# Kernel tuning notes

Measured on AMD Instinct MI355X. Metric: run time of the kernel, lower is better.

The kernel has to match this reference:

```python
import jax, jax.numpy as jnp
import numpy as np

N, E, F_IN, H, T, G, NCONV = 50000, 800000, 128, 64, 8, 64, 3
BN_EPS = 1e-5


def _bn_relu(h, gamma, beta):
    # BatchNorm1d in training mode: biased batch stats over the node dim
    m = h.mean(axis=0)
    v = h.var(axis=0)
    return jax.nn.relu(gamma * (h - m) * jax.lax.rsqrt(v + BN_EPS) + beta)


def _mlp(h, W1, b1, g1, be1, W2, b2, g2, be2):
    h = _bn_relu(h @ W1 + b1, g1, be1)
    return _bn_relu(h @ W2 + b2, g2, be2)


def setup_inputs() -> dict:
    key = jax.random.key(0)
    ks = jax.random.split(key, 12)
    x = jax.random.normal(ks[0], (N, F_IN), dtype=jnp.float32)
    edge_index = jax.random.randint(ks[1], (2, E), 0, N, dtype=jnp.int64)
    batch = jnp.sort(jax.random.randint(ks[2], (N,), 0, G, dtype=jnp.int64))
    s = 0.05
    inp = {
        "x": x, "edge_index": edge_index, "batch": batch,
        # first_h: Linear(F_IN,H)+BN+ReLU+Linear(H,H)+BN+ReLU
        "fh_W1": jax.random.normal(ks[3], (F_IN, H), jnp.float32) * s,
        "fh_b1": jnp.zeros((H,), jnp.float32),
        "fh_g1": jnp.ones((H,), jnp.float32),
        "fh_be1": jnp.zeros((H,), jnp.float32),
        "fh_W2": jax.random.normal(ks[4], (H, H), jnp.float32) * s,
        "fh_b2": jnp.zeros((H,), jnp.float32),
        "fh_g2": jnp.ones((H,), jnp.float32),
        "fh_be2": jnp.zeros((H,), jnp.float32),
        # stacked GINConv MLPs (all H->H)
        "cv_W1": jax.random.normal(ks[5], (NCONV, H, H), jnp.float32) * s,
        "cv_b1": jnp.zeros((NCONV, H), jnp.float32),
        "cv_g1": jnp.ones((NCONV, H), jnp.float32),
        "cv_be1": jnp.zeros((NCONV, H), jnp.float32),
        "cv_W2": jax.random.normal(ks[6], (NCONV, H, H), jnp.float32) * s,
        "cv_b2": jnp.zeros((NCONV, H), jnp.float32),
        "cv_g2": jnp.ones((NCONV, H), jnp.float32),
        "cv_be2": jnp.zeros((NCONV, H), jnp.float32),
        # per-layer readout linears (NCONV+1 of them)
        "lin_W": jax.random.normal(ks[7], (NCONV + 1, H, T), jnp.float32) * s,
        "lin_b": jnp.zeros((NCONV + 1, T), jnp.float32),
    }
    return inp


def reference(x, edge_index, batch, fh_W1, fh_b1, fh_g1, fh_be1, fh_W2, fh_b2,
              fh_g2, fh_be2, cv_W1, cv_b1, cv_g1, cv_be1, cv_W2, cv_b2, cv_g2,
              cv_be2, lin_W, lin_b):
    src, dst = edge_index[0], edge_index[1]
    eps = 0.0  # eps=0.0, train_eps=False
    # layer 0: first_h + pooled readout
    h = _mlp(x, fh_W1, fh_b1, fh_g1, fh_be1, fh_W2, fh_b2, fh_g2, fh_be2)
    out = jax.ops.segment_max(h @ lin_W[0] + lin_b[0], batch, num_segments=G)
    # GIN conv layers: neighbor sum-aggregation + MLP, with per-layer readout
    for l in range(NCONV):
        agg = jax.ops.segment_sum(h[src], dst, num_segments=N)  # [N,H]
        h = _mlp((1.0 + eps) * h + agg, cv_W1[l], cv_b1[l], cv_g1[l],
                 cv_be1[l], cv_W2[l], cv_b2[l], cv_g2[l], cv_be2[l])
        out = out + jax.ops.segment_max(h @ lin_W[l + 1] + lin_b[l + 1],
                                        batch, num_segments=G)
    return (out, h)
```

## Files before the change

kernel.cpp:

```cpp
#include <hip/hip_runtime.h>
#include <hip/hip_fp16.h>

#define NN 50000
#define EE 800000
#define FIN 128
#define HH 64
#define TT 8
#define GG 64
#define NCONVS 3
#define BN_EPS 1e-5f
#define RNODES 128
#define NBKT 196
#define SCAT_CHUNK 2048

__device__ __forceinline__ unsigned enc_f32(float x) {
  unsigned u = __float_as_uint(x);
  return (u & 0x80000000u) ? ~u : (u | 0x80000000u);
}
__device__ __forceinline__ float dec_f32(unsigned e) {
  unsigned u = (e & 0x80000000u) ? (e & 0x7fffffffu) : ~e;
  return __uint_as_float(u);
}

template <int K, int MODE>
__global__ __launch_bounds__(256) void mm_stats_kernel(
    const float* __restrict__ in, const __half* __restrict__ hin,
    const float* __restrict__ agg, const float* __restrict__ stats_in,
    const float* __restrict__ gamma, const float* __restrict__ beta,
    const float* __restrict__ W, const float* __restrict__ bias,
    __half* __restrict__ y16, float* __restrict__ stats_out) {
  __shared__ float Wl[K * HH];
  __shared__ float Al[16][K + 1];
  __shared__ float ssl[128];
  __shared__ float sred[4][128];
  const int t = threadIdx.x;
  {
    const float4* W4 = (const float4*)W;
    float4* Wl4 = (float4*)Wl;
#pragma unroll
    for (int i = 0; i < (K * HH) / 1024; ++i) Wl4[t + i * 256] = W4[t + i * 256];
  }
  if (MODE == 1 && t < 64) {
    const float inv = 1.f / (float)NN;
    const float mean = stats_in[t] * inv;
    const float var = stats_in[64 + t] * inv - mean * mean;
    const float sc = gamma[t] * rsqrtf(var + BN_EPS);
    ssl[t] = sc;
    ssl[64 + t] = fmaf(-mean, sc, beta[t]);
  }
  const int r = t >> 4, g = t & 15;
  const float4 bb = *(const float4*)&bias[g * 4];
  float st_s[4] = {0.f, 0.f, 0.f, 0.f}, st_q[4] = {0.f, 0.f, 0.f, 0.f};
  __syncthreads();

#pragma unroll
  for (int chunk = 0; chunk < 4; ++chunk) {
    const int row = blockIdx.x * 64 + chunk * 16 + r;
    if (row < NN) {
      if (MODE == 0) {
#pragma unroll
        for (int p = 0; p < K / 64; ++p) {
          const int c0 = g * 4 + p * 64;
          const float4 v = *(const float4*)&in[row * K + c0];
          Al[r][c0 + 0] = v.x; Al[r][c0 + 1] = v.y;
          Al[r][c0 + 2] = v.z; Al[r][c0 + 3] = v.w;
        }
      } else if (MODE == 1) {
        const int c0 = g * 4;
        const int2 hraw = *(const int2*)&hin[row * HH + c0];
        const float2 f0 = __half22float2(*(const __half2*)&hraw.x);
        const float2 f1 = __half22float2(*(const __half2*)&hraw.y);
        Al[r][c0 + 0] = fmaxf(fmaf(f0.x, ssl[c0 + 0], ssl[64 + c0 + 0]), 0.f);
        Al[r][c0 + 1] = fmaxf(fmaf(f0.y, ssl[c0 + 1], ssl[64 + c0 + 1]), 0.f);
        Al[r][c0 + 2] = fmaxf(fmaf(f1.x, ssl[c0 + 2], ssl[64 + c0 + 2]), 0.f);
        Al[r][c0 + 3] = fmaxf(fmaf(f1.y, ssl[c0 + 3], ssl[64 + c0 + 3]), 0.f);
      } else {
        const int c0 = g * 4;
        const int2 hraw = *(const int2*)&hin[row * HH + c0];
        const float2 f0 = __half22float2(*(const __half2*)&hraw.x);
        const float2 f1 = __half22float2(*(const __half2*)&hraw.y);
        const float4 a = *(const float4*)&agg[row * HH + c0];
        Al[r][c0 + 0] = f0.x + a.x; Al[r][c0 + 1] = f0.y + a.y;
        Al[r][c0 + 2] = f1.x + a.z; Al[r][c0 + 3] = f1.y + a.w;
      }
    } else {
#pragma unroll
      for (int p = 0; p < K / 64; ++p) {
        const int c0 = g * 4 + p * 64;
        Al[r][c0 + 0] = 0.f; Al[r][c0 + 1] = 0.f;
        Al[r][c0 + 2] = 0.f; Al[r][c0 + 3] = 0.f;
      }
    }
    __syncthreads();
    float ax = 0.f, ay = 0.f, az = 0.f, aw = 0.f;
#pragma unroll
    for (int k = 0; k < K; ++k) {
      const float a = Al[r][k];
      const float4 w = *(const float4*)&Wl[k * HH + g * 4];
      ax = fmaf(a, w.x, ax); ay = fmaf(a, w.y, ay);
      az = fmaf(a, w.z, az); aw = fmaf(a, w.w, aw);
    }
    if (row < NN) {
      float4 o;
      o.x = ax + bb.x; o.y = ay + bb.y; o.z = az + bb.z; o.w = aw + bb.w;
      const __half2 p0 = __floats2half2_rn(o.x, o.y);
      const __half2 p1 = __floats2half2_rn(o.z, o.w);
      int2 pk;
      pk.x = *(const int*)&p0; pk.y = *(const int*)&p1;
      *(int2*)&y16[row * HH + g * 4] = pk;
      st_s[0] += o.x; st_s[1] += o.y; st_s[2] += o.z; st_s[3] += o.w;
      st_q[0] = fmaf(o.x, o.x, st_q[0]); st_q[1] = fmaf(o.y, o.y, st_q[1]);
      st_q[2] = fmaf(o.z, o.z, st_q[2]); st_q[3] = fmaf(o.w, o.w, st_q[3]);
    }
    __syncthreads();
  }
#pragma unroll
  for (int off = 16; off <= 32; off <<= 1) {
#pragma unroll
    for (int i = 0; i < 4; ++i) {
      st_s[i] += __shfl_xor(st_s[i], off);
      st_q[i] += __shfl_xor(st_q[i], off);
    }
  }
  const int wave = t >> 6, lane = t & 63;
  if (lane < 16) {
#pragma unroll
    for (int i = 0; i < 4; ++i) {
      sred[wave][lane * 4 + i] = st_s[i];
      sred[wave][64 + lane * 4 + i] = st_q[i];
    }
  }
  __syncthreads();
  if (t < 128)
    atomicAdd(&stats_out[t],
              sred[0][t] + sred[1][t] + sred[2][t] + sred[3][t]);
}

__global__ __launch_bounds__(256) void bcount_kernel(const int* __restrict__ ei,
                                                     int* __restrict__ bcnt) {
  __shared__ int l[256];
  const int t = threadIdx.x;
  l[t] = 0;
  __syncthreads();
  for (int e = blockIdx.x * 256 + t; e < EE; e += gridDim.x * 256)
    atomicAdd(&l[ei[EE + e] >> 8], 1);
  __syncthreads();
  if (t < NBKT && l[t]) atomicAdd(&bcnt[t], l[t]);
}

__global__ void bscan_kernel(const int* __restrict__ bcnt,
                             int* __restrict__ bbase, int* __restrict__ bcur) {
  __shared__ int s[256];
  const int t = threadIdx.x;
  const int v = (t < NBKT) ? bcnt[t] : 0;
  s[t] = v;
  __syncthreads();
  for (int off = 1; off < 256; off <<= 1) {
    const int u = (t >= off) ? s[t - off] : 0;
    __syncthreads();
    s[t] += u;
    __syncthreads();
  }
  const int excl = s[t] - v;
  if (t < NBKT) {
    bbase[t] = excl;
    bcur[t] = excl;
  }
  if (t == 255) bbase[NBKT] = s[255];
}

__global__ __launch_bounds__(256) void bscatter_kernel(
    const int* __restrict__ ei, int* __restrict__ bcur,
    unsigned long long* __restrict__ ebuf) {
  __shared__ int lcnt[256];
  __shared__ int lbase[256];
  const int t = threadIdx.x;
  lcnt[t] = 0;
  __syncthreads();
  const int e0 = blockIdx.x * SCAT_CHUNK;
  int mysrc[8], mydl[8], mybkt[8], myloc[8];
#pragma unroll
  for (int i = 0; i < 8; ++i) {
    const int e = e0 + i * 256 + t;
    if (e < EE) {
      const int dst = ei[EE + e];
      mybkt[i] = dst >> 8;
      mydl[i] = dst & 255;
      mysrc[i] = ei[e];
      myloc[i] = atomicAdd(&lcnt[mybkt[i]], 1);
    } else {
      mybkt[i] = -1;
    }
  }
  __syncthreads();
  if (t < NBKT && lcnt[t]) lbase[t] = atomicAdd(&bcur[t], lcnt[t]);
  __syncthreads();
#pragma unroll
  for (int i = 0; i < 8; ++i) {
    if (mybkt[i] >= 0) {
      const int pos = lbase[mybkt[i]] + myloc[i];
      ebuf[pos] = ((unsigned long long)(unsigned)mydl[i] << 32) |
                  (unsigned)mysrc[i];
    }
  }
}

__global__ __launch_bounds__(256) void bcsr_kernel(
    const int* __restrict__ bbase, const unsigned long long* __restrict__ ebuf,
    int* __restrict__ offs, int* __restrict__ srcs) {
  __shared__ int ldeg[256];
  __shared__ int sscan[256];
  __shared__ int lcur[256];
  const int t = threadIdx.x;
  const int b = blockIdx.x;
  const int e0 = bbase[b], e1 = bbase[b + 1];
  ldeg[t] = 0;
  __syncthreads();
  for (int e = e0 + t; e < e1; e += 256)
    atomicAdd(&ldeg[(int)(ebuf[e] >> 32)], 1);
  __syncthreads();
  const int v = ldeg[t];
  sscan[t] = v;
  __syncthreads();
  for (int off = 1; off < 256; off <<= 1) {
    const int u = (t >= off) ? sscan[t - off] : 0;
    __syncthreads();
    sscan[t] += u;
    __syncthreads();
  }
  const int excl = sscan[t] - v;
  const int node = b * 256 + t;
  if (node < NN) offs[node] = e0 + excl;
  if (b == NBKT - 1 && t == 0) offs[NN] = EE;
  lcur[t] = e0 + excl;
  __syncthreads();
  for (int e = e0 + t; e < e1; e += 256) {
    const unsigned long long u = ebuf[e];
    const int dl = (int)(u >> 32);
    const int pos = atomicAdd(&lcur[dl], 1);
    srcs[pos] = (int)(u & 0xffffffffu);
  }
}

__device__ __forceinline__ void acc_half8(const int4 r, float4& lo, float4& hi) {
  const __half2* p = (const __half2*)&r;
  const float2 f0 = __half22float2(p[0]);
  const float2 f1 = __half22float2(p[1]);
  const float2 f2 = __half22float2(p[2]);
  const float2 f3 = __half22float2(p[3]);
  lo.x += f0.x; lo.y += f0.y; lo.z += f1.x; lo.w += f1.y;
  hi.x += f2.x; hi.y += f2.y; hi.z += f3.x; hi.w += f3.y;
}

__global__ __launch_bounds__(256) void gather16_kernel(
    const int* __restrict__ offs, const int* __restrict__ srcs,
    const __half* __restrict__ h16, float* __restrict__ agg) {
  const int gid = blockIdx.x * 256 + threadIdx.x;
  const int n = gid >> 3, lane = gid & 7;
  if (n >= NN) return;
  const int c0 = lane * 8;
  const int s0 = offs[n], s1 = offs[n + 1];
  float4 aA0 = make_float4(0, 0, 0, 0), aA1 = make_float4(0, 0, 0, 0);
  float4 aB0 = make_float4(0, 0, 0, 0), aB1 = make_float4(0, 0, 0, 0);
  int j = s0;
  for (; j + 1 < s1; j += 2) {
    const int sA = srcs[j], sB = srcs[j + 1];
    const int4 rA = *(const int4*)&h16[sA * HH + c0];
    const int4 rB = *(const int4*)&h16[sB * HH + c0];
    acc_half8(rA, aA0, aA1);
    acc_half8(rB, aB0, aB1);
  }
  if (j < s1) {
    const int4 rA = *(const int4*)&h16[srcs[j] * HH + c0];
    acc_half8(rA, aA0, aA1);
  }
  aA0.x += aB0.x; aA0.y += aB0.y; aA0.z += aB0.z; aA0.w += aB0.w;
  aA1.x += aB1.x; aA1.y += aB1.y; aA1.z += aB1.z; aA1.w += aB1.w;
  *(float4*)&agg[n * HH + c0] = aA0;
  *(float4*)&agg[n * HH + c0 + 4] = aA1;
}

template <int WMODE>
__global__ __launch_bounds__(256) void bnrelu_readout_kernel(
    const __half* __restrict__ y2, const float* __restrict__ stats_in,
    const float* __restrict__ gamma, const float* __restrict__ beta,
    float* __restrict__ hout, __half* __restrict__ h16out,
    const float* __restrict__ linW, const float* __restrict__ linb,
    const int* __restrict__ batch, unsigned* __restrict__ outmax) {
  __shared__ float Wl[HH * 9];
  __shared__ float lb[8];
  __shared__ float ssl[128];
  __shared__ unsigned smax[8][8];
  const int t = threadIdx.x;
  if (t < 64) {
#pragma unroll
    for (int j = 0; j < 8; ++j) Wl[t * 9 + j] = linW[t * 8 + j];
    const float inv = 1.f / (float)NN;
    const float mean = stats_in[t] * inv;
    const float var = stats_in[64 + t] * inv - mean * mean;
    const float sc = gamma[t] * rsqrtf(var + BN_EPS);
    ssl[t] = sc;
    ssl[64 + t] = fmaf(-mean, sc, beta[t]);
  }
  if (t < 8) lb[t] = linb[t];
  if (t >= 64 && t < 128) smax[(t - 64) >> 3][(t - 64) & 7] = 0u;
  const int gfirst = batch[blockIdx.x * RNODES < NN ? blockIdx.x * RNODES : NN - 1];
  __syncthreads();
  const int nl = t >> 3;
  const int c0 = (t & 7) * 8;
  const int b0 = t & 1, b1 = (t >> 1) & 1, b2 = (t >> 2) & 1;
#pragma unroll
  for (int chunk = 0; chunk < RNODES / 32; ++chunk) {
    const int n = blockIdx.x * RNODES + chunk * 32 + nl;
    if (n < NN) {
      float hv[8];
      {
        const int4 rv = *(const int4*)&y2[n * HH + c0];
        const __half2* hp = (const __half2*)&rv;
        const float2 f0 = __half22float2(hp[0]);
        const float2 f1 = __half22float2(hp[1]);
        const float2 f2 = __half22float2(hp[2]);
        const float2 f3 = __half22float2(hp[3]);
        hv[0] = fmaxf(fmaf(f0.x, ssl[c0 + 0], ssl[64 + c0 + 0]), 0.f);
        hv[1] = fmaxf(fmaf(f0.y, ssl[c0 + 1], ssl[64 + c0 + 1]), 0.f);
        hv[2] = fmaxf(fmaf(f1.x, ssl[c0 + 2], ssl[64 + c0 + 2]), 0.f);
        hv[3] = fmaxf(fmaf(f1.y, ssl[c0 + 3], ssl[64 + c0 + 3]), 0.f);
        hv[4] = fmaxf(fmaf(f2.x, ssl[c0 + 4], ssl[64 + c0 + 4]), 0.f);
        hv[5] = fmaxf(fmaf(f2.y, ssl[c0 + 5], ssl[64 + c0 + 5]), 0.f);
        hv[6] = fmaxf(fmaf(f3.x, ssl[c0 + 6], ssl[64 + c0 + 6]), 0.f);
        hv[7] = fmaxf(fmaf(f3.y, ssl[c0 + 7], ssl[64 + c0 + 7]), 0.f);
      }
      if (WMODE == 1) {
        *(float4*)&hout[n * HH + c0] = make_float4(hv[0], hv[1], hv[2], hv[3]);
        *(float4*)&hout[n * HH + c0 + 4] = make_float4(hv[4], hv[5], hv[6], hv[7]);
      } else {
        const __half2 p0 = __floats2half2_rn(hv[0], hv[1]);
        const __half2 p1 = __floats2half2_rn(hv[2], hv[3]);
        const __half2 p2 = __floats2half2_rn(hv[4], hv[5]);
        const __half2 p3 = __floats2half2_rn(hv[6], hv[7]);
        int4 pk;
        pk.x = *(const int*)&p0; pk.y = *(const int*)&p1;
        pk.z = *(const int*)&p2; pk.w = *(const int*)&p3;
        *(int4*)&h16out[n * HH + c0] = pk;
      }
      float rr[8] = {0, 0, 0, 0, 0, 0, 0, 0};
#pragma unroll
      for (int j = 0; j < 8; ++j) {
        const float a = hv[j];
        const int k = c0 + j;
#pragma unroll
        for (int u = 0; u < 8; ++u) rr[u] = fmaf(a, Wl[k * 9 + u], rr[u]);
      }
      float s4[4];
#pragma unroll
      for (int i = 0; i < 4; ++i) {
        const float keepv = b0 ? rr[2 * i + 1] : rr[2 * i];
        const float send = b0 ? rr[2 * i] : rr[2 * i + 1];
        s4[i] = keepv + __shfl_xor(send, 1);
      }
      float s2[2];
#pragma unroll
      for (int i = 0; i < 2; ++i) {
        const float keepv = b1 ? s4[2 * i + 1] : s4[2 * i];
        const float send = b1 ? s4[2 * i] : s4[2 * i + 1];
        s2[i] = keepv + __shfl_xor(send, 2);
      }
      const float keepv = b2 ? s2[1] : s2[0];
      const float send = b2 ? s2[0] : s2[1];
      const float v = keepv + __shfl_xor(send, 4) + lb[t & 7];
      const int g = batch[n];
      const int gidx = g - gfirst;
      const unsigned ev = enc_f32(v);
      if (gidx < 8)
        atomicMax(&smax[gidx][t & 7], ev);
      else
        atomicMax(&outmax[g * 8 + (t & 7)], ev);
    }
  }
  __syncthreads();
  if (t < 64) {
    const unsigned vv = smax[t >> 3][t & 7];
    if (vv) atomicMax(&outmax[(gfirst + (t >> 3)) * 8 + (t & 7)], vv);
  }
}

__global__ void combine_kernel(const unsigned* __restrict__ outmax,
                               float* __restrict__ out) {
  const int i = blockIdx.x * 64 + threadIdx.x;
  float s = 0.f;
#pragma unroll
  for (int l = 0; l < 4; ++l) s += dec_f32(outmax[l * GG * TT + i]);
  out[i] = s;
}

extern "C" void kernel_launch(void* const* d_in, const int* in_sizes, int n_in,
                              void* d_out, int out_size, void* d_ws,
                              size_t ws_size, hipStream_t stream) {
  const float* x      = (const float*)d_in[0];
  const int*   ei     = (const int*)d_in[1];
  const int*   batch  = (const int*)d_in[2];
  const float* fh_W1  = (const float*)d_in[3];
  const float* fh_b1  = (const float*)d_in[4];
  const float* fh_g1  = (const float*)d_in[5];
  const float* fh_be1 = (const float*)d_in[6];
  const float* fh_W2  = (const float*)d_in[7];
  const float* fh_b2  = (const float*)d_in[8];
  const float* fh_g2  = (const float*)d_in[9];
  const float* fh_be2 = (const float*)d_in[10];
  const float* cv_W1  = (const float*)d_in[11];
  const float* cv_b1  = (const float*)d_in[12];
  const float* cv_g1  = (const float*)d_in[13];
  const float* cv_be1 = (const float*)d_in[14];
  const float* cv_W2  = (const float*)d_in[15];
  const float* cv_b2  = (const float*)d_in[16];
  const float* cv_g2  = (const float*)d_in[17];
  const float* cv_be2 = (const float*)d_in[18];
  const float* lin_W  = (const float*)d_in[19];
  const float* lin_b  = (const float*)d_in[20];

  float* out = (float*)d_out;
  float* h = out + GG * TT;

  char* w = (char*)d_ws;
  float* stats = (float*)w;                       w += 8 * 128 * 4;
  unsigned* outmax = (unsigned*)w;                w += 4 * GG * TT * 4;
  int* bcnt = (int*)w;                            w += 256 * 4;
  int* bbase = (int*)w;                           w += 256 * 4;
  int* bcur = (int*)w;                            w += 256 * 4;
  int* offs = (int*)w;                            w += (NN + 1) * 4;
  int* srcs = (int*)w;                            w += (size_t)EE * 4;
  w = (char*)(((size_t)w + 15) & ~(size_t)15);
  __half* h16 = (__half*)w;                       w += (size_t)NN * HH * 2;
  __half* y1 = (__half*)w;                        w += (size_t)NN * HH * 2;
  __half* y2 = (__half*)w;                        w += (size_t)NN * HH * 2;
  w = (char*)(((size_t)w + 15) & ~(size_t)15);
  float* agg = (float*)w;                         w += (size_t)NN * HH * 4;
  unsigned long long* ebuf = (unsigned long long*)agg;

  const int NBLK = (NN + 63) / 64;
  const int NRD = (NN + RNODES - 1) / RNODES;
  const int NGA = (NN * 8 + 255) / 256;
  const int NSC = (EE + SCAT_CHUNK - 1) / SCAT_CHUNK;

  hipMemsetAsync(stats, 0, (8 * 128 + 4 * GG * TT) * sizeof(float), stream);
  hipMemsetAsync(bcnt, 0, 256 * sizeof(int), stream);

  bcount_kernel<<<512, 256, 0, stream>>>(ei, bcnt);
  bscan_kernel<<<1, 256, 0, stream>>>(bcnt, bbase, bcur);
  bscatter_kernel<<<NSC, 256, 0, stream>>>(ei, bcur, ebuf);
  bcsr_kernel<<<NBKT, 256, 0, stream>>>(bbase, ebuf, offs, srcs);

  mm_stats_kernel<FIN, 0><<<NBLK, 256, 0, stream>>>(
      x, nullptr, nullptr, nullptr, nullptr, nullptr, fh_W1, fh_b1, y1, stats);
  mm_stats_kernel<HH, 1><<<NBLK, 256, 0, stream>>>(
      nullptr, y1, nullptr, stats, fh_g1, fh_be1, fh_W2, fh_b2, y2, stats + 128);
  bnrelu_readout_kernel<0><<<NRD, 256, 0, stream>>>(
      y2, stats + 128, fh_g2, fh_be2, h, h16, lin_W, lin_b, batch, outmax);

  for (int l = 0; l < NCONVS; ++l) {
    float* s1 = stats + (2 + 2 * l) * 128;
    float* s2 = stats + (3 + 2 * l) * 128;
    gather16_kernel<<<NGA, 256, 0, stream>>>(offs, srcs, h16, agg);
    mm_stats_kernel<HH, 2><<<NBLK, 256, 0, stream>>>(
        nullptr, h16, agg, nullptr, nullptr, nullptr,
        cv_W1 + l * HH * HH, cv_b1 + l * HH, y1, s1);
    mm_stats_kernel<HH, 1><<<NBLK, 256, 0, stream>>>(
        nullptr, y1, nullptr, s1, cv_g1 + l * HH, cv_be1 + l * HH,
        cv_W2 + l * HH * HH, cv_b2 + l * HH, y2, s2);
    if (l == NCONVS - 1) {
      bnrelu_readout_kernel<1><<<NRD, 256, 0, stream>>>(
          y2, s2, cv_g2 + l * HH, cv_be2 + l * HH, h, h16,
          lin_W + (l + 1) * HH * TT, lin_b + (l + 1) * TT, batch,
          outmax + (l + 1) * GG * TT);
    } else {
      bnrelu_readout_kernel<0><<<NRD, 256, 0, stream>>>(
          y2, s2, cv_g2 + l * HH, cv_be2 + l * HH, h, h16,
          lin_W + (l + 1) * HH * TT, lin_b + (l + 1) * TT, batch,
          outmax + (l + 1) * GG * TT);
    }
  }
  combine_kernel<<<8, 64, 0, stream>>>(outmax, out);
}
```

Before: 407.1 us.

## Register-tile matmul with transposed LDS staging and store aggregation in fp16

The fused matmul+stats kernel now computes a 4x4 output tile per thread. A is staged once per 64-wide K phase into a transposed, padded LDS buffer, which replaces the four 16-row chunks, each with its own barriers and LDS reads. This raises FMA-per-LDS-load reuse and removes most synchronisation. Separately, the neighbour aggregation buffer is written and read as fp16 instead of fp32, halving that round-trip traffic in every conv layer at some cost in accumulation precision.

```diff
diff --git a/kernel.cpp b/kernel.cpp
--- a/kernel.cpp
+++ b/kernel.cpp
@@ -25,94 +25,126 @@
 template <int K, int MODE>
 __global__ __launch_bounds__(256) void mm_stats_kernel(
     const float* __restrict__ in, const __half* __restrict__ hin,
-    const float* __restrict__ agg, const float* __restrict__ stats_in,
+    const __half* __restrict__ agg, const float* __restrict__ stats_in,
     const float* __restrict__ gamma, const float* __restrict__ beta,
     const float* __restrict__ W, const float* __restrict__ bias,
     __half* __restrict__ y16, float* __restrict__ stats_out) {
+  constexpr int NPH = K / 64;
   __shared__ float Wl[K * HH];
-  __shared__ float Al[16][K + 1];
+  __shared__ float AT[64 * 68];
   __shared__ float ssl[128];
   __shared__ float sred[4][128];
   const int t = threadIdx.x;
+  if (MODE == 1) {
+    if (t < 64) {
+      const float inv = 1.f / (float)NN;
+      const float mean = stats_in[t] * inv;
+      const float var = stats_in[64 + t] * inv - mean * mean;
+      const float sc = gamma[t] * rsqrtf(var + BN_EPS);
+      ssl[t] = sc;
+      ssl[64 + t] = fmaf(-mean, sc, beta[t]);
+    }
+    __syncthreads();
+  }
   {
     const float4* W4 = (const float4*)W;
     float4* Wl4 = (float4*)Wl;
 #pragma unroll
     for (int i = 0; i < (K * HH) / 1024; ++i) Wl4[t + i * 256] = W4[t + i * 256];
   }
-  if (MODE == 1 && t < 64) {
-    const float inv = 1.f / (float)NN;
-    const float mean = stats_in[t] * inv;
-    const float var = stats_in[64 + t] * inv - mean * mean;
-    const float sc = gamma[t] * rsqrtf(var + BN_EPS);
-    ssl[t] = sc;
-    ssl[64 + t] = fmaf(-mean, sc, beta[t]);
-  }
-  const int r = t >> 4, g = t & 15;
-  const float4 bb = *(const float4*)&bias[g * 4];
+  const int srow = t >> 2, scq = t & 3;
+  const int grow_s = blockIdx.x * 64 + srow;
+  const int g4 = (t & 15) * 4;
+  const int r0 = (t >> 4) * 4;
+  const int row0 = blockIdx.x * 64 + r0;
+  const float4 bb = *(const float4*)&bias[g4];
+  float4 acc0 = make_float4(0, 0, 0, 0), acc1 = make_float4(0, 0, 0, 0);
+  float4 acc2 = make_float4(0, 0, 0, 0), acc3 = make_float4(0, 0, 0, 0);
+
+#pragma unroll
+  for (int p = 0; p < NPH; ++p) {
+    if (p > 0) __syncthreads();
+    if (MODE == 0) {
+      if (grow_s < NN) {
+#pragma unroll
+        for (int i = 0; i < 4; ++i) {
+          const int kl = scq * 16 + i * 4;
+          const float4 v = *(const float4*)&in[(size_t)grow_s * K + p * 64 + kl];
+          AT[(kl + 0) * 68 + srow] = v.x;
+          AT[(kl + 1) * 68 + srow] = v.y;
+          AT[(kl + 2) * 68 + srow] = v.z;
+          AT[(kl + 3) * 68 + srow] = v.w;
+        }
+      } else {
+#pragma unroll
+        for (int i = 0; i < 16; ++i) AT[(scq * 16 + i) * 68 + srow] = 0.f;
+      }
+    } else {
+      if (grow_s < NN) {
+#pragma unroll
+        for (int q = 0; q < 2; ++q) {
+          const int kl = scq * 16 + q * 8;
+          const int4 rv = *(const int4*)&hin[grow_s * HH + kl];
+          const __half2* hp = (const __half2*)&rv;
+          const float2 f0 = __half22float2(hp[0]);
+          const float2 f1 = __half22float2(hp[1]);
+          const float2 f2 = __half22float2(hp[2]);
+          const float2 f3 = __half22float2(hp[3]);
+          float f[8] = {f0.x, f0.y, f1.x, f1.y, f2.x, f2.y, f3.x, f3.y};
+          if (MODE == 2) {
+            const int4 av = *(const int4*)&agg[grow_s * HH + kl];
+            const __half2* ap = (const __half2*)&av;
+            const float2 a0 = __half22float2(ap[0]);
+            const float2 a1 = __half22float2(ap[1]);
+            const float2 a2 = __half22float2(ap[2]);
+            const float2 a3 = __half22float2(ap[3]);
+            f[0] += a0.x; f[1] += a0.y; f[2] += a1.x; f[3] += a1.y;
+            f[4] += a2.x; f[5] += a2.y; f[6] += a3.x; f[7] += a3.y;
+          } else {
+#pragma unroll
+            for (int j = 0; j < 8; ++j)
+              f[j] = fmaxf(fmaf(f[j], ssl[kl + j], ssl[64 + kl + j]), 0.f);
+          }
+#pragma unroll
+          for (int j = 0; j < 8; ++j) AT[(kl + j) * 68 + srow] = f[j];
+        }
+      } else {
+#pragma unroll
+        for (int i = 0; i < 16; ++i) AT[(scq * 16 + i) * 68 + srow] = 0.f;
+      }
+    }
+    __syncthreads();
+#pragma unroll 8
+    for (int kl = 0; kl < 64; ++kl) {
+      const float4 w = *(const float4*)&Wl[(p * 64 + kl) * HH + g4];
+      const float4 a = *(const float4*)&AT[kl * 68 + r0];
+      acc0.x = fmaf(a.x, w.x, acc0.x); acc0.y = fmaf(a.x, w.y, acc0.y);
+      acc0.z = fmaf(a.x, w.z, acc0.z); acc0.w = fmaf(a.x, w.w, acc0.w);
+      acc1.x = fmaf(a.y, w.x, acc1.x); acc1.y = fmaf(a.y, w.y, acc1.y);
+      acc1.z = fmaf(a.y, w.z, acc1.z); acc1.w = fmaf(a.y, w.w, acc1.w);
+      acc2.x = fmaf(a.z, w.x, acc2.x); acc2.y = fmaf(a.z, w.y, acc2.y);
+      acc2.z = fmaf(a.z, w.z, acc2.z); acc2.w = fmaf(a.z, w.w, acc2.w);
+      acc3.x = fmaf(a.w, w.x, acc3.x); acc3.y = fmaf(a.w, w.y, acc3.y);
+      acc3.z = fmaf(a.w, w.z, acc3.z); acc3.w = fmaf(a.w, w.w, acc3.w);
+    }
+  }
   float st_s[4] = {0.f, 0.f, 0.f, 0.f}, st_q[4] = {0.f, 0.f, 0.f, 0.f};
-  __syncthreads();
-
-#pragma unroll
-  for (int chunk = 0; chunk < 4; ++chunk) {
-    const int row = blockIdx.x * 64 + chunk * 16 + r;
-    if (row < NN) {
-      if (MODE == 0) {
-#pragma unroll
-        for (int p = 0; p < K / 64; ++p) {
-          const int c0 = g * 4 + p * 64;
-          const float4 v = *(const float4*)&in[row * K + c0];
-          Al[r][c0 + 0] = v.x; Al[r][c0 + 1] = v.y;
-          Al[r][c0 + 2] = v.z; Al[r][c0 + 3] = v.w;
-        }
-      } else if (MODE == 1) {
-        const int c0 = g * 4;
-        const int2 hraw = *(const int2*)&hin[row * HH + c0];
-        const float2 f0 = __half22float2(*(const __half2*)&hraw.x);
-        const float2 f1 = __half22float2(*(const __half2*)&hraw.y);
-        Al[r][c0 + 0] = fmaxf(fmaf(f0.x, ssl[c0 + 0], ssl[64 + c0 + 0]), 0.f);
-        Al[r][c0 + 1] = fmaxf(fmaf(f0.y, ssl[c0 + 1], ssl[64 + c0 + 1]), 0.f);
-        Al[r][c0 + 2] = fmaxf(fmaf(f1.x, ssl[c0 + 2], ssl[64 + c0 + 2]), 0.f);
-        Al[r][c0 + 3] = fmaxf(fmaf(f1.y, ssl[c0 + 3], ssl[64 + c0 + 3]), 0.f);
-      } else {
-        const int c0 = g * 4;
-        const int2 hraw = *(const int2*)&hin[row * HH + c0];
-        const float2 f0 = __half22float2(*(const __half2*)&hraw.x);
-        const float2 f1 = __half22float2(*(const __half2*)&hraw.y);
-        const float4 a = *(const float4*)&agg[row * HH + c0];
-        Al[r][c0 + 0] = f0.x + a.x; Al[r][c0 + 1] = f0.y + a.y;
-        Al[r][c0 + 2] = f1.x + a.z; Al[r][c0 + 3] = f1.y + a.w;
-      }
-    } else {
-#pragma unroll
-      for (int p = 0; p < K / 64; ++p) {
-        const int c0 = g * 4 + p * 64;
-        Al[r][c0 + 0] = 0.f; Al[r][c0 + 1] = 0.f;
-        Al[r][c0 + 2] = 0.f; Al[r][c0 + 3] = 0.f;
-      }
-    }
-    __syncthreads();
-    float ax = 0.f, ay = 0.f, az = 0.f, aw = 0.f;
-#pragma unroll
-    for (int k = 0; k < K; ++k) {
-      const float a = Al[r][k];
-      const float4 w = *(const float4*)&Wl[k * HH + g * 4];
-      ax = fmaf(a, w.x, ax); ay = fmaf(a, w.y, ay);
-      az = fmaf(a, w.z, az); aw = fmaf(a, w.w, aw);
-    }
-    if (row < NN) {
+#pragma unroll
+  for (int ri = 0; ri < 4; ++ri) {
+    const int grow = row0 + ri;
+    if (grow < NN) {
+      const float4 ac = (ri == 0) ? acc0 : (ri == 1) ? acc1 : (ri == 2) ? acc2 : acc3;
       float4 o;
-      o.x = ax + bb.x; o.y = ay + bb.y; o.z = az + bb.z; o.w = aw + bb.w;
+      o.x = ac.x + bb.x; o.y = ac.y + bb.y; o.z = ac.z + bb.z; o.w = ac.w + bb.w;
       const __half2 p0 = __floats2half2_rn(o.x, o.y);
       const __half2 p1 = __floats2half2_rn(o.z, o.w);
       int2 pk;
       pk.x = *(const int*)&p0; pk.y = *(const int*)&p1;
-      *(int2*)&y16[row * HH + g * 4] = pk;
+      *(int2*)&y16[grow * HH + g4] = pk;
       st_s[0] += o.x; st_s[1] += o.y; st_s[2] += o.z; st_s[3] += o.w;
       st_q[0] = fmaf(o.x, o.x, st_q[0]); st_q[1] = fmaf(o.y, o.y, st_q[1]);
       st_q[2] = fmaf(o.z, o.z, st_q[2]); st_q[3] = fmaf(o.w, o.w, st_q[3]);
     }
-    __syncthreads();
   }
 #pragma unroll
   for (int off = 16; off <= 32; off <<= 1) {
@@ -254,7 +286,7 @@
 
 __global__ __launch_bounds__(256) void gather16_kernel(
     const int* __restrict__ offs, const int* __restrict__ srcs,
-    const __half* __restrict__ h16, float* __restrict__ agg) {
+    const __half* __restrict__ h16, __half* __restrict__ agg) {
   const int gid = blockIdx.x * 256 + threadIdx.x;
   const int n = gid >> 3, lane = gid & 7;
   if (n >= NN) return;
@@ -276,8 +308,14 @@
   }
   aA0.x += aB0.x; aA0.y += aB0.y; aA0.z += aB0.z; aA0.w += aB0.w;
   aA1.x += aB1.x; aA1.y += aB1.y; aA1.z += aB1.z; aA1.w += aB1.w;
-  *(float4*)&agg[n * HH + c0] = aA0;
-  *(float4*)&agg[n * HH + c0 + 4] = aA1;
+  const __half2 p0 = __floats2half2_rn(aA0.x, aA0.y);
+  const __half2 p1 = __floats2half2_rn(aA0.z, aA0.w);
+  const __half2 p2 = __floats2half2_rn(aA1.x, aA1.y);
+  const __half2 p3 = __floats2half2_rn(aA1.z, aA1.w);
+  int4 pk;
+  pk.x = *(const int*)&p0; pk.y = *(const int*)&p1;
+  pk.z = *(const int*)&p2; pk.w = *(const int*)&p3;
+  *(int4*)&agg[n * HH + c0] = pk;
 }
 
 template <int WMODE>
@@ -434,7 +472,7 @@
   __half* y1 = (__half*)w;                        w += (size_t)NN * HH * 2;
   __half* y2 = (__half*)w;                        w += (size_t)NN * HH * 2;
   w = (char*)(((size_t)w + 15) & ~(size_t)15);
-  float* agg = (float*)w;                         w += (size_t)NN * HH * 4;
+  __half* agg = (__half*)w;                       w += (size_t)NN * HH * 2;
   unsigned long long* ebuf = (unsigned long long*)agg;
 
   const int NBLK = (NN + 63) / 64;
```

Result: faster. 362.3 us (-11.0%).
